# Kernel tuning notes

Measured on AMD Instinct MI355X. Metric: run time of the kernel, lower is better.

The kernel has to match this reference:

```python
import jax, jax.numpy as jnp
import numpy as np

B, N, C = 2, 9216, 512
HEAD, SR = 8, 4
R = 32  # lora rank
SCALING = 4.0 / 32.0  # alpha / r


def setup_inputs() -> dict:
    key = jax.random.key(0)
    ks = jax.random.split(key, 16)
    s = 0.02
    inp = {
        "x": jax.random.normal(ks[0], (B, N, C), jnp.float32),
        "w_q": jax.random.normal(ks[1], (C, C), jnp.float32) * s,
        "b_q": jnp.zeros((C,), jnp.float32),
        "w_kv": jax.random.normal(ks[2], (2 * C, C), jnp.float32) * s,
        "b_kv": jnp.zeros((2 * C,), jnp.float32),
        "w_proj": jax.random.normal(ks[3], (C, C), jnp.float32) * s,
        "b_proj": jnp.zeros((C,), jnp.float32),
        "w_sr": jax.random.normal(ks[4], (C, C, SR, SR), jnp.float32) * s,
        "b_sr": jnp.zeros((C,), jnp.float32),
        "ln_g": jnp.ones((C,), jnp.float32),
        "ln_b": jnp.zeros((C,), jnp.float32),
        "lora_A_q": jax.random.normal(ks[5], (R, C), jnp.float32) * s,
        "lora_B_q": jax.random.normal(ks[6], (C, R), jnp.float32) * s,
        "lora_A_v": jax.random.normal(ks[7], (R, C), jnp.float32) * s,
        "lora_B_v": jax.random.normal(ks[8], (C, R), jnp.float32) * s,
        "H": 96,
        "W": 96,
    }
    return inp


def reference(x, w_q, b_q, w_kv, b_kv, w_proj, b_proj, w_sr, b_sr,
              ln_g, ln_b, lora_A_q, lora_B_q, lora_A_v, lora_B_v, H, W):
    b, n, c = x.shape
    d = c // HEAD
    # q = Linear(x) + LoRA(x) * scaling
    q = x @ w_q.T + b_q + ((x @ lora_A_q.T) @ lora_B_q.T) * SCALING
    q = q.reshape(b, n, HEAD, d).transpose(0, 2, 1, 3)  # (B, h, N, d)
    # spatial reduction: Conv2d(dim, dim, sr, sr) then LayerNorm
    xi = x.transpose(0, 2, 1).reshape(b, c, H, W)
    xs = jax.lax.conv_general_dilated(
        xi, w_sr, window_strides=(SR, SR), padding='VALID',
        dimension_numbers=('NCHW', 'OIHW', 'NCHW'))
    xs = xs + b_sr[None, :, None, None]
    xs = xs.reshape(b, c, -1).transpose(0, 2, 1)  # (B, Nkv, C)
    mu = jnp.mean(xs, axis=-1, keepdims=True)
    var = jnp.var(xs, axis=-1, keepdims=True)
    xs = (xs - mu) * jax.lax.rsqrt(var + 1e-5) * ln_g + ln_b
    # k, v
    kv = (xs @ w_kv.T + b_kv).reshape(b, -1, 2, HEAD, d).transpose(2, 0, 3, 1, 4)
    k, v = kv[0], kv[1]  # (B, h, Nkv, d)
    lv = ((xs @ lora_A_v.T) @ lora_B_v.T) * SCALING  # (B, Nkv, C)
    # faithful to torch: raw memory reshape, NOT a head-transpose
    v = v + lv.reshape(b, HEAD, -1, d)
    # attention
    attn = jax.nn.softmax(jnp.einsum('bhnd,bhmd->bhnm', q, k) * (d ** -0.5), axis=-1)
    out = jnp.einsum('bhnm,bhmd->bhnd', attn, v).transpose(0, 2, 1, 3).reshape(b, n, c)
    return out @ w_proj.T + b_proj
```

## Files before the change

### kernel.cpp

```cpp
#include <hip/hip_runtime.h>

typedef __attribute__((ext_vector_type(8))) __bf16 bf16x8;
typedef __attribute__((ext_vector_type(4))) float f32x4;
typedef __attribute__((ext_vector_type(4))) unsigned int u32x4;
typedef __attribute__((ext_vector_type(2))) unsigned int u32x2;

#define MFMA16(a, b, c) __builtin_amdgcn_mfma_f32_16x16x32_bf16((a), (b), (c), 0, 0, 0)
#define QSCALE 0.18033688011112042f

__device__ __forceinline__ bool input_is_f32(const void* ln_g) {
    return ((const unsigned*)ln_g)[0] == 0x3F800000u;
}

__device__ __forceinline__ float rdf(const void* p, long i, bool f32) {
    return f32 ? ((const float*)p)[i] : (float)((const __bf16*)p)[i];
}

__device__ __forceinline__ void conv_big(const void* s, __bf16* d, long base, bool f) {
    long i = base + (long)threadIdx.x * 8;
    if (f) {
        f32x4 a = ((const f32x4*)s)[i / 4];
        f32x4 b = ((const f32x4*)s)[i / 4 + 1];
        bf16x8 o;
        #pragma unroll
        for (int j = 0; j < 4; ++j) { o[j] = (__bf16)a[j]; o[4 + j] = (__bf16)b[j]; }
        *(bf16x8*)(d + i) = o;
    } else {
        *(u32x4*)(d + i) = ((const u32x4*)s)[i / 8];
    }
}

__device__ __forceinline__ void conv_small(const void* s, __bf16* d, int n, bool f) {
    int i = threadIdx.x * 4;
    if (i < n) {
        #pragma unroll
        for (int j = 0; j < 4; ++j)
            d[i + j] = f ? (__bf16)((const float*)s)[i + j] : ((const __bf16*)s)[i + j];
    }
}

__global__ void convert_prep_kernel(const void* x, const void* w_kv, const void* w_proj,
                                    const void* b_q, const void* b_kv, const void* b_proj,
                                    const void* b_sr, const void* ln_g, const void* ln_b,
                                    const void* __restrict__ w_q,
                                    const void* __restrict__ Aq, const void* __restrict__ Bq,
                                    const void* __restrict__ Av, const void* __restrict__ Bv,
                                    const void* __restrict__ w_sr,
                                    __bf16* x_b, __bf16* w_kv_b, __bf16* w_proj_b,
                                    __bf16* b_q_b, __bf16* b_kv_b, __bf16* b_proj_b,
                                    __bf16* b_sr_b, __bf16* ln_g_b, __bf16* ln_b_b,
                                    __bf16* __restrict__ w_q_eff, __bf16* __restrict__ w_lv,
                                    __bf16* __restrict__ w_sr_t) {
    const bool f = input_is_f32(ln_g);
    int blk = blockIdx.x;
    if (blk < 4608)      conv_big(x, x_b, (long)blk * 2048, f);
    else if (blk < 4864) conv_big(w_kv, w_kv_b, (long)(blk - 4608) * 2048, f);
    else if (blk < 4992) conv_big(w_proj, w_proj_b, (long)(blk - 4864) * 2048, f);
    else if (blk == 4992) conv_small(b_q, b_q_b, 512, f);
    else if (blk == 4993) conv_small(b_kv, b_kv_b, 1024, f);
    else if (blk == 4994) conv_small(b_proj, b_proj_b, 512, f);
    else if (blk == 4995) conv_small(b_sr, b_sr_b, 512, f);
    else if (blk == 4996) conv_small(ln_g, ln_g_b, 512, f);
    else if (blk == 4997) conv_small(ln_b, ln_b_b, 512, f);
    else {
        int tid = (blk - 4998) * 256 + threadIdx.x;
        if (tid < 262144) {
            int o = tid >> 9, c = tid & 511;
            float acc = 0.f;
            #pragma unroll 8
            for (int r = 0; r < 32; ++r)
                acc += rdf(Bq, o * 32 + r, f) * rdf(Aq, r * 512 + c, f);
            w_q_eff[tid] = (__bf16)(rdf(w_q, tid, f) + 0.125f * acc);
        } else if (tid < 524288) {
            int t = tid - 262144;
            int o = t >> 9, c = t & 511;
            float acc = 0.f;
            #pragma unroll 8
            for (int r = 0; r < 32; ++r)
                acc += rdf(Bv, o * 32 + r, f) * rdf(Av, r * 512 + c, f);
            w_lv[t] = (__bf16)(0.125f * acc);
        } else if (tid < 786432) {
            int t = tid - 524288;
            int o = t >> 9, i = t & 511;
            #pragma unroll
            for (int p = 0; p < 16; ++p)
                w_sr_t[(size_t)o * 8192 + p * 512 + i] = (__bf16)rdf(w_sr, (long)t * 16 + p, f);
        }
    }
}

__global__ __launch_bounds__(256, 2) void qconv_gemm(const __bf16* __restrict__ x,
                                                     const __bf16* __restrict__ Wt,
                                                     const __bf16* __restrict__ Wq,
                                                     const __bf16* __restrict__ bq,
                                                     float* __restrict__ part,
                                                     __bf16* __restrict__ q_t) {
    __shared__ __attribute__((aligned(16))) char lds[36864];
    char* As = lds;
    char* Bs = lds + 18432;
    const int tid = threadIdx.x;
    const int blk = blockIdx.x;
    const bool isconv = blk < 576;
    const int w = tid >> 6, lane = tid & 63;
    const int wm = (w >> 1) << 6, wn = (w & 1) << 6;
    const int lr = lane & 15, lg = lane >> 4;
    const int srow = tid >> 1, half = tid & 1;

    int m0, n0, kzv = 0;
    const __bf16 *Arow, *Brow;
    if (isconv) {
        int mb = blk % 9;
        int rest = blk / 9;
        int nb = rest & 3;
        kzv = rest >> 2;
        m0 = mb << 7; n0 = nb << 7;
        int m = m0 + srow;
        int bb = m >= 576 ? 1 : 0;
        int rem = m - bb * 576;
        int oy = rem / 24;
        int ox = rem - oy * 24;
        int ky = kzv >> 2, kx = kzv & 3;
        Arow = x + ((size_t)bb * 9216 + (size_t)(oy * 384 + ky * 96 + ox * 4 + kx)) * 512
               + half * 32;
        Brow = Wt + (size_t)(n0 + srow) * 8192 + kzv * 512 + half * 32;
    } else {
        int b2 = blk - 576;
        int mb = b2 % 144, nb = b2 / 144;
        m0 = mb << 7; n0 = nb << 7;
        Arow = x + (size_t)(m0 + srow) * 512 + half * 32;
        Brow = Wq + (size_t)(n0 + srow) * 512 + half * 32;
    }
    char* Asw = As + srow * 144 + half * 64;
    char* Bsw = Bs + srow * 144 + half * 64;

    f32x4 acc[4][4] = {};

    u32x4 a0 = *(const u32x4*)(Arow);
    u32x4 a1 = *(const u32x4*)(Arow + 8);
    u32x4 a2 = *(const u32x4*)(Arow + 16);
    u32x4 a3 = *(const u32x4*)(Arow + 24);
    u32x4 b0 = *(const u32x4*)(Brow);
    u32x4 b1 = *(const u32x4*)(Brow + 8);
    u32x4 b2 = *(const u32x4*)(Brow + 16);
    u32x4 b3 = *(const u32x4*)(Brow + 24);

    for (int k0 = 0; k0 < 512; k0 += 64) {
        __syncthreads();
        *(u32x4*)(Asw) = a0;
        *(u32x4*)(Asw + 16) = a1;
        *(u32x4*)(Asw + 32) = a2;
        *(u32x4*)(Asw + 48) = a3;
        *(u32x4*)(Bsw) = b0;
        *(u32x4*)(Bsw + 16) = b1;
        *(u32x4*)(Bsw + 32) = b2;
        *(u32x4*)(Bsw + 48) = b3;
        __syncthreads();
        int kn = k0 + 64;
        if (kn < 512) {
            a0 = *(const u32x4*)(Arow + kn);
            a1 = *(const u32x4*)(Arow + kn + 8);
            a2 = *(const u32x4*)(Arow + kn + 16);
            a3 = *(const u32x4*)(Arow + kn + 24);
            b0 = *(const u32x4*)(Brow + kn);
            b1 = *(const u32x4*)(Brow + kn + 8);
            b2 = *(const u32x4*)(Brow + kn + 16);
            b3 = *(const u32x4*)(Brow + kn + 24);
        }
        bf16x8 a[4][2], b[4][2];
        #pragma unroll
        for (int i = 0; i < 4; ++i)
            #pragma unroll
            for (int ks = 0; ks < 2; ++ks)
                a[i][ks] = *(const bf16x8*)(As + (wm + i * 16 + lr) * 144 + ks * 64 + lg * 16);
        #pragma unroll
        for (int j = 0; j < 4; ++j)
            #pragma unroll
            for (int ks = 0; ks < 2; ++ks)
                b[j][ks] = *(const bf16x8*)(Bs + (wn + j * 16 + lr) * 144 + ks * 64 + lg * 16);
        #pragma unroll
        for (int i = 0; i < 4; ++i)
            #pragma unroll
            for (int j = 0; j < 4; ++j)
                #pragma unroll
                for (int ks = 0; ks < 2; ++ks)
                    acc[i][j] = MFMA16(a[i][ks], b[j][ks], acc[i][j]);
    }

    if (isconv) {
        float* pout = part + (size_t)kzv * 589824;
        #pragma unroll
        for (int j = 0; j < 4; ++j) {
            int col = n0 + wn + j * 16 + lr;
            #pragma unroll
            for (int i = 0; i < 4; ++i) {
                int rb = m0 + wm + i * 16 + lg * 4;
                #pragma unroll
                for (int r = 0; r < 4; ++r)
                    pout[(size_t)(rb + r) * 512 + col] = acc[i][j][r];
            }
        }
    } else {
        #pragma unroll
        for (int j = 0; j < 4; ++j) {
            int col = n0 + wn + j * 16 + lr;
            float bv = (float)bq[col];
            #pragma unroll
            for (int i = 0; i < 4; ++i) {
                int rb = m0 + wm + i * 16 + lg * 4;
                #pragma unroll
                for (int r = 0; r < 4; ++r) {
                    int grow = rb + r;
                    int b_ = grow >= 9216 ? 1 : 0;
                    int nn = grow - b_ * 9216;
                    q_t[(((size_t)(b_ * 8 + (col >> 6))) * 9216 + nn) * 64 + (col & 63)] =
                        (__bf16)((acc[i][j][r] + bv) * QSCALE);
                }
            }
        }
    }
}

__global__ __launch_bounds__(256, 2) void proj_gemm(const __bf16* __restrict__ A,
                                                    const __bf16* __restrict__ Bt,
                                                    const __bf16* __restrict__ bias,
                                                    float* __restrict__ out) {
    __shared__ __attribute__((aligned(16))) char lds[27648];
    char* As = lds;
    char* Bs = lds + 9216;
    const int tid = threadIdx.x;
    const int m0 = blockIdx.x << 6, n0 = blockIdx.y << 7;
    const int w = tid >> 6, lane = tid & 63;
    const int wm = (w >> 1) << 5, wn = (w & 1) << 6;
    const int lr = lane & 15, lg = lane >> 4;

    f32x4 acc[2][4] = {};

    const int srow = tid >> 1, half = tid & 1;
    const bool doA = tid < 128;
    const __bf16* Arow = A + (size_t)(m0 + (srow & 63)) * 512 + half * 32;
    const __bf16* Brow = Bt + (size_t)(n0 + srow) * 512 + half * 32;
    char* Asw = As + (srow & 63) * 144 + half * 64;
    char* Bsw = Bs + srow * 144 + half * 64;

    u32x4 a0{}, a1{}, a2{}, a3{};
    if (doA) {
        a0 = *(const u32x4*)(Arow);
        a1 = *(const u32x4*)(Arow + 8);
        a2 = *(const u32x4*)(Arow + 16);
        a3 = *(const u32x4*)(Arow + 24);
    }
    u32x4 b0 = *(const u32x4*)(Brow);
    u32x4 b1 = *(const u32x4*)(Brow + 8);
    u32x4 b2 = *(const u32x4*)(Brow + 16);
    u32x4 b3 = *(const u32x4*)(Brow + 24);

    for (int k0 = 0; k0 < 512; k0 += 64) {
        __syncthreads();
        if (doA) {
            *(u32x4*)(Asw) = a0;
            *(u32x4*)(Asw + 16) = a1;
            *(u32x4*)(Asw + 32) = a2;
            *(u32x4*)(Asw + 48) = a3;
        }
        *(u32x4*)(Bsw) = b0;
        *(u32x4*)(Bsw + 16) = b1;
        *(u32x4*)(Bsw + 32) = b2;
        *(u32x4*)(Bsw + 48) = b3;
        __syncthreads();
        int kn = k0 + 64;
        if (kn < 512) {
            if (doA) {
                a0 = *(const u32x4*)(Arow + kn);
                a1 = *(const u32x4*)(Arow + kn + 8);
                a2 = *(const u32x4*)(Arow + kn + 16);
                a3 = *(const u32x4*)(Arow + kn + 24);
            }
            b0 = *(const u32x4*)(Brow + kn);
            b1 = *(const u32x4*)(Brow + kn + 8);
            b2 = *(const u32x4*)(Brow + kn + 16);
            b3 = *(const u32x4*)(Brow + kn + 24);
        }
        bf16x8 a[2][2], b[4][2];
        #pragma unroll
        for (int i = 0; i < 2; ++i)
            #pragma unroll
            for (int ks = 0; ks < 2; ++ks)
                a[i][ks] = *(const bf16x8*)(As + (wm + i * 16 + lr) * 144 + ks * 64 + lg * 16);
        #pragma unroll
        for (int j = 0; j < 4; ++j)
            #pragma unroll
            for (int ks = 0; ks < 2; ++ks)
                b[j][ks] = *(const bf16x8*)(Bs + (wn + j * 16 + lr) * 144 + ks * 64 + lg * 16);
        #pragma unroll
        for (int i = 0; i < 2; ++i)
            #pragma unroll
            for (int j = 0; j < 4; ++j)
                #pragma unroll
                for (int ks = 0; ks < 2; ++ks)
                    acc[i][j] = MFMA16(a[i][ks], b[j][ks], acc[i][j]);
    }

    #pragma unroll
    for (int j = 0; j < 4; ++j) {
        int col = n0 + wn + j * 16 + lr;
        float bv = (float)bias[col];
        #pragma unroll
        for (int i = 0; i < 2; ++i) {
            int rb = m0 + wm + i * 16 + lg * 4;
            #pragma unroll
            for (int r = 0; r < 4; ++r)
                out[(size_t)(rb + r) * 512 + col] = acc[i][j][r] + bv;
        }
    }
}

__global__ __launch_bounds__(64) void lnorm(const float* __restrict__ parts,
                                            const __bf16* __restrict__ b_sr,
                                            const __bf16* __restrict__ g,
                                            const __bf16* __restrict__ be,
                                            __bf16* __restrict__ out) {
    int row = blockIdx.x;
    int lane = threadIdx.x;
    const float* xr = parts + (size_t)row * 512;
    float v[8], s = 0.f, sq = 0.f;
    #pragma unroll
    for (int i = 0; i < 8; ++i) {
        int c = lane + i * 64;
        float t = (float)b_sr[c];
        #pragma unroll
        for (int sp = 0; sp < 16; ++sp)
            t += xr[(size_t)sp * 589824 + c];
        v[i] = t;
        s += t;
        sq += t * t;
    }
    #pragma unroll
    for (int d = 1; d < 64; d <<= 1) {
        s += __shfl_xor(s, d);
        sq += __shfl_xor(sq, d);
    }
    float mean = s * (1.0f / 512.0f);
    float var = sq * (1.0f / 512.0f) - mean * mean;
    float rstd = rsqrtf(var + 1e-5f);
    __bf16* orow = out + (size_t)row * 512;
    #pragma unroll
    for (int i = 0; i < 8; ++i) {
        int c = lane + i * 64;
        orow[c] = (__bf16)((v[i] - mean) * rstd * (float)g[c] + (float)be[c]);
    }
}

__global__ __launch_bounds__(256) void kv_gemm(const __bf16* __restrict__ xs,
                                               const __bf16* __restrict__ w_kv,
                                               const __bf16* __restrict__ w_lv,
                                               const __bf16* __restrict__ b_kv,
                                               __bf16* __restrict__ k_t,
                                               float* __restrict__ v_raw,
                                               __bf16* __restrict__ lv) {
    __shared__ __attribute__((aligned(16))) char lds[18432];
    char* As = lds;
    char* Bs = lds + 9216;
    const int tid = threadIdx.x;
    const int m0 = blockIdx.x << 6, n0 = blockIdx.y << 6;
    const int w = tid >> 6, lane = tid & 63;
    const int wm = (w >> 1) << 5, wn = (w & 1) << 5;
    const int lr = lane & 15, lg = lane >> 4;

    const int srow = tid >> 2, sc = tid & 3;
    const __bf16* arow = xs + (size_t)(m0 + srow) * 512;
    const __bf16* brow = (n0 < 1024) ? (w_kv + (size_t)(n0 + srow) * 512)
                                     : (w_lv + (size_t)(n0 - 1024 + srow) * 512);

    u32x4 pav[2], pbv[2];
    #pragma unroll
    for (int j = 0; j < 2; ++j) {
        int c = sc + j * 4;
        pav[j] = *(const u32x4*)(arow + c * 8);
        pbv[j] = *(const u32x4*)(brow + c * 8);
    }

    f32x4 acc[2][2] = {};
    for (int k0 = 0; k0 < 512; k0 += 64) {
        __syncthreads();
        #pragma unroll
        for (int j = 0; j < 2; ++j) {
            int c = sc + j * 4;
            *(u32x4*)(As + srow * 144 + c * 16) = pav[j];
            *(u32x4*)(Bs + srow * 144 + c * 16) = pbv[j];
        }
        __syncthreads();
        int kn = k0 + 64;
        if (kn < 512) {
            #pragma unroll
            for (int j = 0; j < 2; ++j) {
                int c = sc + j * 4;
                pav[j] = *(const u32x4*)(arow + kn + c * 8);
                pbv[j] = *(const u32x4*)(brow + kn + c * 8);
            }
        }
        bf16x8 a[2][2], b[2][2];
        #pragma unroll
        for (int i = 0; i < 2; ++i)
            #pragma unroll
            for (int ks = 0; ks < 2; ++ks) {
                a[i][ks] = *(const bf16x8*)(As + (wm + i * 16 + lr) * 144 + ks * 64 + lg * 16);
                b[i][ks] = *(const bf16x8*)(Bs + (wn + i * 16 + lr) * 144 + ks * 64 + lg * 16);
            }
        #pragma unroll
        for (int i = 0; i < 2; ++i)
            #pragma unroll
            for (int j = 0; j < 2; ++j)
                #pragma unroll
                for (int ks = 0; ks < 2; ++ks)
                    acc[i][j] = MFMA16(a[i][ks], b[j][ks], acc[i][j]);
    }
    #pragma unroll
    for (int j = 0; j < 2; ++j) {
        int col = n0 + wn + j * 16 + lr;
        float bv = (col < 1024) ? (float)b_kv[col] : 0.0f;
        #pragma unroll
        for (int i = 0; i < 2; ++i) {
            int rb = m0 + wm + i * 16 + lg * 4;
            #pragma unroll
            for (int r = 0; r < 4; ++r) {
                int grow = rb + r;
                float val = acc[i][j][r] + bv;
                int b_ = grow >= 576 ? 1 : 0;
                int mm = grow - b_ * 576;
                if (col < 512) {
                    int h = col >> 6, dd = col & 63;
                    k_t[(((size_t)(b_ * 8 + h)) * 576 + mm) * 64 + dd] = (__bf16)val;
                } else if (col < 1024) {
                    v_raw[((size_t)b_ * 576 + mm) * 512 + (col - 512)] = val;
                } else {
                    lv[((size_t)b_ * 576 + mm) * 512 + (col - 1024)] = (__bf16)val;
                }
            }
        }
    }
}

__global__ void v_fixup(const float* __restrict__ v_raw, const __bf16* __restrict__ lv,
                        __bf16* __restrict__ vT) {
    int tid = blockIdx.x * 256 + threadIdx.x;
    if (tid >= 589824) return;
    int mm = tid % 576;
    int rest = tid / 576;
    int dd = rest & 63;
    int bh = rest >> 6;
    int b_ = bh >> 3, h = bh & 7;
    int flat = h * 36864 + mm * 64 + dd;
    int n2 = flat >> 9, c2 = flat & 511;
    float val = v_raw[((size_t)b_ * 576 + mm) * 512 + h * 64 + dd] +
                (float)lv[((size_t)b_ * 576 + n2) * 512 + c2];
    vT[tid] = (__bf16)val;
}

__global__ __launch_bounds__(256, 2) void attn_kernel(const __bf16* __restrict__ q_t,
                                                      const __bf16* __restrict__ k_t,
                                                      const __bf16* __restrict__ vT,
                                                      __bf16* __restrict__ attnv) {
    __shared__ __attribute__((aligned(16))) char lds[18432];
    char* Ks = lds;
    char* Vs = lds + 9216;
    const int tid = threadIdx.x;
    const int w = tid >> 6, lane = tid & 63;
    const int lr = lane & 15, lg = lane >> 4;
    const int bh = blockIdx.y;
    const int qrow0 = (blockIdx.x << 8) + (w << 6);

    bf16x8 qf[4][2];
    #pragma unroll
    for (int qb = 0; qb < 4; ++qb)
        #pragma unroll
        for (int ks = 0; ks < 2; ++ks)
            qf[qb][ks] = *(const bf16x8*)(q_t + ((size_t)bh * 9216 + qrow0 + qb * 16 + lr) * 64 +
                                          ks * 32 + lg * 8);

    bf16x8 ones;
    #pragma unroll
    for (int j = 0; j < 8; ++j) ones[j] = (__bf16)1.0f;

    f32x4 oacc[4][4] = {};
    f32x4 lacc[4] = {};

    const int rr = tid >> 2, q4 = tid & 3;
    const __bf16* kg = k_t + ((size_t)bh * 576 + rr) * 64 + q4 * 16;
    char* ksw = Ks + rr * 144 + q4 * 32;
    const __bf16* vg = vT + ((size_t)bh * 64 + rr) * 576 + q4 * 16;
    char* vsw = Vs + rr * 144;
    const int offA = ((q4 & 1) << 3) | ((q4 >> 1) << 6);

    u32x4 k0v = *(const u32x4*)(kg);
    u32x4 k1v = *(const u32x4*)(kg + 8);
    u32x4 v0v = *(const u32x4*)(vg);
    u32x4 v1v = *(const u32x4*)(vg + 8);

    for (int kv0 = 0; kv0 < 576; kv0 += 64) {
        __syncthreads();
        *(u32x4*)(ksw) = k0v;
        *(u32x4*)(ksw + 16) = k1v;
        {
            u32x2 t0, t1, t2, t3;
            t0[0] = v0v[0]; t0[1] = v0v[1];
            t1[0] = v0v[2]; t1[1] = v0v[3];
            t2[0] = v1v[0]; t2[1] = v1v[1];
            t3[0] = v1v[2]; t3[1] = v1v[3];
            *(u32x2*)(vsw + offA) = t0;
            *(u32x2*)(vsw + offA + 16) = t1;
            *(u32x2*)(vsw + offA + 32) = t2;
            *(u32x2*)(vsw + offA + 48) = t3;
        }
        __syncthreads();
        int kvn = kv0 + 64;
        if (kvn < 576) {
            k0v = *(const u32x4*)(kg + (size_t)kvn * 64);
            k1v = *(const u32x4*)(kg + (size_t)kvn * 64 + 8);
            v0v = *(const u32x4*)(vg + kvn);
            v1v = *(const u32x4*)(vg + kvn + 8);
        }

        #pragma unroll
        for (int ch = 0; ch < 2; ++ch) {
            bf16x8 kf[2][2];
            #pragma unroll
            for (int kb = 0; kb < 2; ++kb)
                #pragma unroll
                for (int ks = 0; ks < 2; ++ks)
                    kf[kb][ks] = *(const bf16x8*)(Ks + ((ch * 2 + kb) * 16 + lr) * 144 +
                                                  ks * 64 + lg * 16);
            f32x4 st[2][4] = {};
            #pragma unroll
            for (int kb = 0; kb < 2; ++kb)
                #pragma unroll
                for (int qb = 0; qb < 4; ++qb)
                    #pragma unroll
                    for (int ks = 0; ks < 2; ++ks)
                        st[kb][qb] = MFMA16(kf[kb][ks], qf[qb][ks], st[kb][qb]);
            bf16x8 vf[4];
            #pragma unroll
            for (int nd = 0; nd < 4; ++nd)
                vf[nd] = *(const bf16x8*)(Vs + (nd * 16 + lr) * 144 + ch * 64 + lg * 16);
            #pragma unroll
            for (int qb = 0; qb < 4; ++qb) {
                bf16x8 pa;
                #pragma unroll
                for (int kb = 0; kb < 2; ++kb)
                    #pragma unroll
                    for (int r = 0; r < 4; ++r)
                        pa[kb * 4 + r] = (__bf16)__builtin_amdgcn_exp2f(st[kb][qb][r]);
                #pragma unroll
                for (int nd = 0; nd < 4; ++nd)
                    oacc[qb][nd] = MFMA16(pa, vf[nd], oacc[qb][nd]);
                lacc[qb] = MFMA16(pa, ones, lacc[qb]);
            }
        }
    }

    const int b_ = bh >> 3, h = bh & 7;
    #pragma unroll
    for (int qb = 0; qb < 4; ++qb) {
        f32x4 linv;
        #pragma unroll
        for (int r = 0; r < 4; ++r) linv[r] = 1.0f / lacc[qb][r];
        #pragma unroll
        for (int nd = 0; nd < 4; ++nd)
            #pragma unroll
            for (int r = 0; r < 4; ++r) {
                int row = qrow0 + qb * 16 + lg * 4 + r;
                int col = h * 64 + nd * 16 + lr;
                attnv[((size_t)b_ * 9216 + row) * 512 + col] =
                    (__bf16)(oacc[qb][nd][r] * linv[r]);
            }
    }
}

extern "C" void kernel_launch(void* const* d_in, const int* in_sizes, int n_in,
                              void* d_out, int out_size, void* d_ws, size_t ws_size,
                              hipStream_t stream) {
    const void* x      = d_in[0];
    const void* w_q    = d_in[1];
    const void* b_q    = d_in[2];
    const void* w_kv   = d_in[3];
    const void* b_kv   = d_in[4];
    const void* w_proj = d_in[5];
    const void* b_proj = d_in[6];
    const void* w_sr   = d_in[7];
    const void* b_sr   = d_in[8];
    const void* ln_g   = d_in[9];
    const void* ln_b   = d_in[10];
    const void* A_q    = d_in[11];
    const void* B_q    = d_in[12];
    const void* A_v    = d_in[13];
    const void* B_v    = d_in[14];

    char* ws = (char*)d_ws;
    __bf16* x_b      = (__bf16*)(ws);
    __bf16* attnv    = (__bf16*)(ws);
    __bf16* q_t      = (__bf16*)(ws + 18874368);
    __bf16* k_t      = (__bf16*)(ws + 37748736);
    __bf16* vT       = (__bf16*)(ws + 38928384);
    __bf16* w_q_eff  = (__bf16*)(ws + 40108032);
    __bf16* w_lv     = (__bf16*)(ws + 40632320);
    __bf16* w_sr_t   = (__bf16*)(ws + 41156608);
    __bf16* w_kv_b   = (__bf16*)(ws + 49545216);
    __bf16* w_proj_b = (__bf16*)(ws + 50593792);
    __bf16* xs_ln    = (__bf16*)(ws + 53477376);
    float*  v_raw    = (float*)(ws + 54657024);
    __bf16* lv       = (__bf16*)(ws + 57016320);
    __bf16* b_q_b    = (__bf16*)(ws + 58195968);
    __bf16* b_kv_b   = (__bf16*)(ws + 58196992);
    __bf16* b_proj_b = (__bf16*)(ws + 58199040);
    __bf16* b_sr_b   = (__bf16*)(ws + 58200064);
    __bf16* ln_g_b   = (__bf16*)(ws + 58201088);
    __bf16* ln_b_b   = (__bf16*)(ws + 58202112);
    float*  parts    = (float*)(ws + 58204160);

    convert_prep_kernel<<<8070, 256, 0, stream>>>(
        x, w_kv, w_proj, b_q, b_kv, b_proj, b_sr, ln_g, ln_b,
        w_q, A_q, B_q, A_v, B_v, w_sr,
        x_b, w_kv_b, w_proj_b, b_q_b, b_kv_b, b_proj_b, b_sr_b, ln_g_b, ln_b_b,
        w_q_eff, w_lv, w_sr_t);
    qconv_gemm<<<1152, 256, 0, stream>>>(x_b, w_sr_t, w_q_eff, b_q_b, parts, q_t);
    lnorm<<<1152, 64, 0, stream>>>(parts, b_sr_b, ln_g_b, ln_b_b, xs_ln);
    kv_gemm<<<dim3(18, 24), 256, 0, stream>>>(xs_ln, w_kv_b, w_lv, b_kv_b, k_t, v_raw, lv);
    v_fixup<<<2304, 256, 0, stream>>>(v_raw, lv, vT);
    attn_kernel<<<dim3(36, 16), 256, 0, stream>>>(q_t, k_t, vT, attnv);
    proj_gemm<<<dim3(288, 4), 256, 0, stream>>>(attnv, w_proj_b, b_proj_b, (float*)d_out);
}
```

Baseline: 259.5 us.

## Reduce conv split-K to four partials, interleave conv/q blocks, swizzle proj grid

```diff
diff --git a/kernel.cpp b/kernel.cpp
--- a/kernel.cpp
+++ b/kernel.cpp
@@ -99,34 +99,35 @@
     char* As = lds;
     char* Bs = lds + 18432;
     const int tid = threadIdx.x;
-    const int blk = blockIdx.x;
-    const bool isconv = blk < 576;
+    const int swz = (blockIdx.x & 7) * 90 + (blockIdx.x >> 3);
+    const int j5 = swz / 5, s5 = swz % 5;
+    const bool isconv = (s5 == 0);
     const int w = tid >> 6, lane = tid & 63;
     const int wm = (w >> 1) << 6, wn = (w & 1) << 6;
     const int lr = lane & 15, lg = lane >> 4;
     const int srow = tid >> 1, half = tid & 1;
 
-    int m0, n0, kzv = 0;
+    int m0, n0, kzv = 0, klen;
     const __bf16 *Arow, *Brow;
     if (isconv) {
-        int mb = blk % 9;
-        int rest = blk / 9;
-        int nb = rest & 3;
-        kzv = rest >> 2;
+        kzv = j5 / 36;
+        int r = j5 % 36;
+        int nb = r / 9, mb = r % 9;
         m0 = mb << 7; n0 = nb << 7;
+        klen = 2048;
         int m = m0 + srow;
         int bb = m >= 576 ? 1 : 0;
         int rem = m - bb * 576;
         int oy = rem / 24;
         int ox = rem - oy * 24;
-        int ky = kzv >> 2, kx = kzv & 3;
-        Arow = x + ((size_t)bb * 9216 + (size_t)(oy * 384 + ky * 96 + ox * 4 + kx)) * 512
+        Arow = x + ((size_t)bb * 9216 + (size_t)(oy * 384 + kzv * 96 + ox * 4)) * 512
                + half * 32;
-        Brow = Wt + (size_t)(n0 + srow) * 8192 + kzv * 512 + half * 32;
+        Brow = Wt + (size_t)(n0 + srow) * 8192 + kzv * 2048 + half * 32;
     } else {
-        int b2 = blk - 576;
-        int mb = b2 % 144, nb = b2 / 144;
+        int qi = j5 * 4 + (s5 - 1);
+        int mb = qi >> 2, nb = qi & 3;
         m0 = mb << 7; n0 = nb << 7;
+        klen = 512;
         Arow = x + (size_t)(m0 + srow) * 512 + half * 32;
         Brow = Wq + (size_t)(n0 + srow) * 512 + half * 32;
     }
@@ -144,7 +145,7 @@
     u32x4 b2 = *(const u32x4*)(Brow + 16);
     u32x4 b3 = *(const u32x4*)(Brow + 24);
 
-    for (int k0 = 0; k0 < 512; k0 += 64) {
+    for (int k0 = 0; k0 < klen; k0 += 64) {
         __syncthreads();
         *(u32x4*)(Asw) = a0;
         *(u32x4*)(Asw + 16) = a1;
@@ -156,7 +157,7 @@
         *(u32x4*)(Bsw + 48) = b3;
         __syncthreads();
         int kn = k0 + 64;
-        if (kn < 512) {
+        if (kn < klen) {
             a0 = *(const u32x4*)(Arow + kn);
             a1 = *(const u32x4*)(Arow + kn + 8);
             a2 = *(const u32x4*)(Arow + kn + 16);
@@ -228,7 +229,8 @@
     char* As = lds;
     char* Bs = lds + 9216;
     const int tid = threadIdx.x;
-    const int m0 = blockIdx.x << 6, n0 = blockIdx.y << 7;
+    const int swz = (blockIdx.x & 7) * 144 + (blockIdx.x >> 3);
+    const int m0 = (swz >> 2) << 6, n0 = (swz & 3) << 7;
     const int w = tid >> 6, lane = tid & 63;
     const int wm = (w >> 1) << 5, wn = (w & 1) << 6;
     const int lr = lane & 15, lg = lane >> 4;
@@ -328,7 +330,7 @@
         int c = lane + i * 64;
         float t = (float)b_sr[c];
         #pragma unroll
-        for (int sp = 0; sp < 16; ++sp)
+        for (int sp = 0; sp < 4; ++sp)
             t += xr[(size_t)sp * 589824 + c];
         v[i] = t;
         s += t;
@@ -621,10 +623,10 @@
         w_q, A_q, B_q, A_v, B_v, w_sr,
         x_b, w_kv_b, w_proj_b, b_q_b, b_kv_b, b_proj_b, b_sr_b, ln_g_b, ln_b_b,
         w_q_eff, w_lv, w_sr_t);
-    qconv_gemm<<<1152, 256, 0, stream>>>(x_b, w_sr_t, w_q_eff, b_q_b, parts, q_t);
+    qconv_gemm<<<720, 256, 0, stream>>>(x_b, w_sr_t, w_q_eff, b_q_b, parts, q_t);
     lnorm<<<1152, 64, 0, stream>>>(parts, b_sr_b, ln_g_b, ln_b_b, xs_ln);
     kv_gemm<<<dim3(18, 24), 256, 0, stream>>>(xs_ln, w_kv_b, w_lv, b_kv_b, k_t, v_raw, lv);
     v_fixup<<<2304, 256, 0, stream>>>(v_raw, lv, vT);
     attn_kernel<<<dim3(36, 16), 256, 0, stream>>>(q_t, k_t, vT, attnv);
-    proj_gemm<<<dim3(288, 4), 256, 0, stream>>>(attnv, w_proj_b, b_proj_b, (float*)d_out);
-}
+    proj_gemm<<<1152, 256, 0, stream>>>(attnv, w_proj_b, b_proj_b, (float*)d_out);
+}
```

After: 247.6 us. 1.05x faster.
